# Optimization experiments

Measured on AMD Instinct MI355X. Metric: run time of the kernel, lower is better.

Reference implementation:

```python
import jax, jax.numpy as jnp
import numpy as np

EPS = 1e-12  # torch F.normalize eps

def setup_inputs() -> dict:
    key = jax.random.key(0)
    k1, k2, k3 = jax.random.split(key, 3)
    N, F_IN, F_OUT = 8192, 512, 256
    adjacency = jax.random.uniform(k1, (N, N), dtype=jnp.float32)
    input_feature = jax.random.normal(k2, (N, F_IN), dtype=jnp.float32)
    # xavier_normal_ with gain=1: std = sqrt(2/(fan_in+fan_out))
    std = float(np.sqrt(2.0 / (F_IN + F_OUT)))
    weight = jax.random.normal(k3, (F_IN, F_OUT), dtype=jnp.float32) * std
    bias = jnp.zeros((F_OUT,), dtype=jnp.float32)
    return {"adjacency": adjacency, "input_feature": input_feature,
            "weight": weight, "bias": bias}

def reference(adjacency, input_feature, weight, bias):
    # row L1 normalization, matching torch.nn.functional.normalize(p=1, dim=1)
    row_norm = jnp.sum(jnp.abs(adjacency), axis=1, keepdims=True)
    adj_n = adjacency / jnp.maximum(row_norm, EPS)
    support = adj_n @ input_feature            # [N, F_in]
    output = support @ weight + bias           # [N, F_out]
    return output
```

## Files before the change

kernel.cpp:

```cpp
#include <hip/hip_runtime.h>
#include <hip/hip_bf16.h>


typedef __attribute__((ext_vector_type(8))) __bf16 bf16x8;
typedef __attribute__((ext_vector_type(4))) float f32x4;

#define AS1 __attribute__((address_space(1)))
#define AS3 __attribute__((address_space(3)))

__device__ __forceinline__ void async_load16(const void* g, void* l) {
  __builtin_amdgcn_global_load_lds((const AS1 void*)g, (AS3 void*)l, 16, 0, 0);
}

__global__ __launch_bounds__(256) void transpose_cvt_kernel(
    const float* __restrict__ src, __hip_bfloat16* __restrict__ dst, int R, int C) {
  __shared__ float tile[64][65];
  const int t = threadIdx.x;
  const int nrb = R >> 6;
  const int rb = blockIdx.x % nrb, cb = blockIdx.x / nrb;
  const int r0 = rb * 64, c0 = cb * 64;
  const int lr = t >> 4, lc4 = (t & 15) * 4;
#pragma unroll
  for (int p = 0; p < 4; ++p) {
    const int r = p * 16 + lr;
    const f32x4 v = *(const f32x4*)(src + (size_t)(r0 + r) * C + c0 + lc4);
    tile[r][lc4 + 0] = v[0]; tile[r][lc4 + 1] = v[1];
    tile[r][lc4 + 2] = v[2]; tile[r][lc4 + 3] = v[3];
  }
  __syncthreads();
#pragma unroll
  for (int i = 0; i < 16; ++i) {
    const int idx = i * 256 + t;
    const int n = idx >> 6, k = idx & 63;
    dst[(size_t)(c0 + n) * R + r0 + k] = __float2bfloat16(tile[k][n]);
  }
}

__global__ __launch_bounds__(256) void gemm_xw_kernel(
    const float* __restrict__ X,
    const __hip_bfloat16* __restrict__ WT,
    __hip_bfloat16* __restrict__ YT)
{
  __shared__ char smem[49152];
  char* Sbase = smem;
  char* Wbase = smem + 16384;

  const int t = threadIdx.x;
  const int wave = t >> 6, lane = t & 63;
  const int quad = lane >> 4, l16 = lane & 15;

  const int b = blockIdx.x;
  const int xcd = b & 7, s = b >> 3;
  const int rb = xcd * 16 + (s >> 1), cb = s & 1;
  const int r0 = rb * 64, c0 = cb * 128;

  const int wm = wave & 1, wn = wave >> 1;

  f32x4 acc[2][4] = {};

  const int am = t >> 2;
  const int kq = t & 3;
  const float* sp = X + (size_t)(r0 + am) * 512 + kq * 16;
  const int sw0 = am * 128 + (((kq * 2 + 0) ^ (am & 7)) * 16);
  const int sw1 = am * 128 + (((kq * 2 + 1) ^ (am & 7)) * 16);

  f32x4 sreg[4];
#pragma unroll
  for (int i = 0; i < 4; ++i) sreg[i] = *(const f32x4*)(sp + i * 4);

#pragma unroll
  for (int i = 0; i < 4; ++i) {
    const int slot = i * 256 + t;
    const int n = slot >> 3;
    const int G = (slot & 7) ^ (n & 7);
    async_load16(WT + (size_t)(c0 + n) * 512 + G * 8, Wbase + slot * 16);
  }

  int cur = 0;
#pragma unroll 2
  for (int kt = 0; kt < 8; ++kt) {
    {
      char* sw = Sbase + cur * 8192;
      bf16x8 v0, v1;
#pragma unroll
      for (int j = 0; j < 4; ++j) {
        v0[j]     = (__bf16)(sreg[0][j]);
        v0[j + 4] = (__bf16)(sreg[1][j]);
        v1[j]     = (__bf16)(sreg[2][j]);
        v1[j + 4] = (__bf16)(sreg[3][j]);
      }
      *(bf16x8*)(sw + sw0) = v0;
      *(bf16x8*)(sw + sw1) = v1;
    }
    __syncthreads();

    if (kt < 7) {
      const float* spk = sp + (kt + 1) * 64;
#pragma unroll
      for (int i = 0; i < 4; ++i) sreg[i] = *(const f32x4*)(spk + i * 4);
#pragma unroll
      for (int i = 0; i < 4; ++i) {
        const int slot = i * 256 + t;
        const int n = slot >> 3;
        const int G = (slot & 7) ^ (n & 7);
        async_load16(WT + (size_t)(c0 + n) * 512 + (kt + 1) * 64 + G * 8,
                     Wbase + (cur ^ 1) * 16384 + slot * 16);
      }
    }

    {
      const char* sb = Sbase + cur * 8192;
      const char* wb = Wbase + cur * 16384;
      bf16x8 af[2][2];
#pragma unroll
      for (int rt = 0; rt < 2; ++rt) {
        const int row = wm * 32 + rt * 16 + l16;
#pragma unroll
        for (int kb = 0; kb < 2; ++kb) {
          const int ch = (kb * 4 + quad) ^ (row & 7);
          af[rt][kb] = *(const bf16x8*)(sb + row * 128 + ch * 16);
        }
      }
#pragma unroll
      for (int ct = 0; ct < 4; ++ct) {
        const int n = wn * 64 + ct * 16 + l16;
#pragma unroll
        for (int kb = 0; kb < 2; ++kb) {
          const int ch = (kb * 4 + quad) ^ (n & 7);
          const bf16x8 bfr = *(const bf16x8*)(wb + n * 128 + ch * 16);
#pragma unroll
          for (int rt = 0; rt < 2; ++rt)
            acc[rt][ct] = __builtin_amdgcn_mfma_f32_16x16x32_bf16(
                af[rt][kb], bfr, acc[rt][ct], 0, 0, 0);
        }
      }
    }
    cur ^= 1;
  }

  __syncthreads();
  __hip_bfloat16* Tr = (__hip_bfloat16*)smem;
#pragma unroll
  for (int rt = 0; rt < 2; ++rt) {
#pragma unroll
    for (int r = 0; r < 4; ++r) {
      const int row_l = wm * 32 + rt * 16 + quad * 4 + r;
#pragma unroll
      for (int ct = 0; ct < 4; ++ct) {
        const int col_l = wn * 64 + ct * 16 + l16;
        Tr[col_l * 64 + row_l] = __float2bfloat16(acc[rt][ct][r]);
      }
    }
  }
  __syncthreads();
#pragma unroll
  for (int i = 0; i < 4; ++i) {
    const int c = i * 256 + t;
    const int col = c >> 3, part = c & 7;
    *(f32x4*)(YT + (size_t)(c0 + col) * 8192 + r0 + part * 8) =
        *(const f32x4*)(Tr + col * 64 + part * 8);
  }
}

__global__ __launch_bounds__(512, 4) void gemm_ay_kernel(
    const float* __restrict__ A,
    const __hip_bfloat16* __restrict__ YT,
    float* __restrict__ Pb,
    float* __restrict__ Rb,
    int atomic_flag)
{
  __shared__ char smem[49152];
  char* Abase = smem;
  char* Ybase = smem + 16384;
  float* rsmem = (float*)Ybase;

  const int t = threadIdx.x;
  const int wave = t >> 6, lane = t & 63;
  const int quad = lane >> 4, l16 = lane & 15;

  const int b = blockIdx.x;
  const int ks = b & 7;
  const int rb = b >> 3;
  const int r0 = rb * 128;
  const int k0 = ks * 1024;

  const int wm = wave & 1, wn = wave >> 1;

  f32x4 acc[4][4] = {};
  float rs = 0.0f;

  const int am = t >> 2;
  const int kc = t & 3;
  const float* ap = A + (size_t)(r0 + am) * 8192 + k0 + kc * 8;
  const int aw_off = (am >> 1) * 128 + (((kc + 4 * (am & 1)) ^ ((am >> 1) & 7)) * 16);

  f32x4 areg[2];
  areg[0] = *(const f32x4*)(ap);
  areg[1] = *(const f32x4*)(ap + 4);

#pragma unroll
  for (int i = 0; i < 2; ++i) {
    const int s = i * 512 + t;
    const int q = s >> 3;
    const int u = (s & 7) ^ (q & 7);
    const int n = 2 * q + (u >> 2), g = u & 3;
    async_load16(YT + (size_t)n * 8192 + k0 + g * 8, Ybase + s * 16);
  }

  int cur = 0;
#pragma unroll 2
  for (int kt = 0; kt < 32; ++kt) {
    {
      const f32x4 e = areg[0], o = areg[1];
      rs += fabsf(e[0]) + fabsf(e[1]) + fabsf(e[2]) + fabsf(e[3]) +
            fabsf(o[0]) + fabsf(o[1]) + fabsf(o[2]) + fabsf(o[3]);
      bf16x8 v;
      v[0] = (__bf16)e[0]; v[1] = (__bf16)e[1]; v[2] = (__bf16)e[2]; v[3] = (__bf16)e[3];
      v[4] = (__bf16)o[0]; v[5] = (__bf16)o[1]; v[6] = (__bf16)o[2]; v[7] = (__bf16)o[3];
      *(bf16x8*)(Abase + cur * 8192 + aw_off) = v;
    }
    __syncthreads();

    if (kt < 31) {
      const float* apk = ap + (kt + 1) * 32;
      areg[0] = *(const f32x4*)(apk);
      areg[1] = *(const f32x4*)(apk + 4);
#pragma unroll
      for (int i = 0; i < 2; ++i) {
        const int s = i * 512 + t;
        const int q = s >> 3;
        const int u = (s & 7) ^ (q & 7);
        const int n = 2 * q + (u >> 2), g = u & 3;
        async_load16(YT + (size_t)n * 8192 + k0 + (kt + 1) * 32 + g * 8,
                     Ybase + (cur ^ 1) * 16384 + s * 16);
      }
    }

    {
      const char* ab = Abase + cur * 8192;
      const char* xb = Ybase + cur * 16384;
      bf16x8 af[4];
#pragma unroll
      for (int rt = 0; rt < 4; ++rt) {
        const int row = wm * 64 + rt * 16 + l16;
        const int off = (row >> 1) * 128 + (((quad + 4 * (row & 1)) ^ ((row >> 1) & 7)) * 16);
        af[rt] = *(const bf16x8*)(ab + off);
      }
#pragma unroll
      for (int ct = 0; ct < 4; ++ct) {
        const int n = wn * 64 + ct * 16 + l16;
        const int off = (n >> 1) * 128 + (((quad + 4 * (n & 1)) ^ ((n >> 1) & 7)) * 16);
        const bf16x8 bfr = *(const bf16x8*)(xb + off);
#pragma unroll
        for (int rt = 0; rt < 4; ++rt)
          acc[rt][ct] = __builtin_amdgcn_mfma_f32_16x16x32_bf16(
              af[rt], bfr, acc[rt][ct], 0, 0, 0);
      }
    }
    cur ^= 1;
  }

  rsmem[t] = rs;
  __syncthreads();
  if (t < 128) {
    const float v = rsmem[4 * t] + rsmem[4 * t + 1] + rsmem[4 * t + 2] + rsmem[4 * t + 3];
    if (atomic_flag) atomicAdd(&Rb[r0 + t], v);
    else             Rb[(size_t)ks * 8192 + r0 + t] = v;
  }

  if (atomic_flag) {
#pragma unroll
    for (int rt = 0; rt < 4; ++rt)
#pragma unroll
      for (int r = 0; r < 4; ++r) {
        const int row_l = wm * 64 + rt * 16 + quad * 4 + r;
#pragma unroll
        for (int ct = 0; ct < 4; ++ct) {
          const int col_l = wn * 64 + ct * 16 + l16;
          atomicAdd(&Pb[(size_t)(r0 + row_l) * 256 + col_l], acc[rt][ct][r]);
        }
      }
  } else {
    float* dst = Pb + (size_t)ks * (8192 * 256);
#pragma unroll
    for (int rt = 0; rt < 4; ++rt)
#pragma unroll
      for (int r = 0; r < 4; ++r) {
        const int row_l = wm * 64 + rt * 16 + quad * 4 + r;
#pragma unroll
        for (int ct = 0; ct < 4; ++ct) {
          const int col_l = wn * 64 + ct * 16 + l16;
          dst[(size_t)(r0 + row_l) * 256 + col_l] = acc[rt][ct][r];
        }
      }
  }
}

__global__ __launch_bounds__(256) void finalize_kernel(
    const float* __restrict__ Pb,
    const float* __restrict__ Rb,
    const float* __restrict__ bias,
    float* __restrict__ Out,
    int S)
{
  const int idx = blockIdx.x * 256 + threadIdx.x;
  const int i  = idx >> 6;
  const int j4 = (idx & 63) << 2;
  float rsum = 0.0f;
  for (int s = 0; s < S; ++s) rsum += Rb[(size_t)s * 8192 + i];
  const float inv = 1.0f / fmaxf(rsum, 1e-12f);
  f32x4 a = {};
  for (int s = 0; s < S; ++s) {
    const f32x4 p = *(const f32x4*)(Pb + (size_t)s * (8192 * 256) + (size_t)i * 256 + j4);
    a += p;
  }
  const f32x4 bv = *(const f32x4*)(bias + j4);
  const f32x4 o = a * inv + bv;
  *(f32x4*)(Out + (size_t)i * 256 + j4) = o;
}

extern "C" void kernel_launch(void* const* d_in, const int* in_sizes, int n_in,
                              void* d_out, int out_size, void* d_ws, size_t ws_size,
                              hipStream_t stream) {
  const float* A    = (const float*)d_in[0];
  const float* Xf   = (const float*)d_in[1];
  const float* Wf   = (const float*)d_in[2];
  const float* bias = (const float*)d_in[3];
  float* Out = (float*)d_out;

  char* ws = (char*)d_ws;
  __hip_bfloat16* WT = (__hip_bfloat16*)ws;
  __hip_bfloat16* YT = (__hip_bfloat16*)(ws + 262144);
  char*         tail = ws + 4456448;

  const size_t need_plain = 4456448ull + 67108864ull + 262144ull;
  float* Pb; float* Rb; int atomic_flag; int S;
  if (ws_size >= need_plain) {
    Pb = (float*)tail;
    Rb = (float*)(tail + 67108864);
    atomic_flag = 0; S = 8;
  } else {
    Pb = (float*)tail;
    Rb = (float*)(tail + 8388608);
    atomic_flag = 1; S = 1;
    hipMemsetAsync(tail, 0, 8388608 + 32768, stream);
  }

  transpose_cvt_kernel<<<32, 256, 0, stream>>>(Wf, WT, 512, 256);
  gemm_xw_kernel<<<256, 256, 0, stream>>>(Xf, WT, YT);
  gemm_ay_kernel<<<512, 512, 0, stream>>>(A, YT, Pb, Rb, atomic_flag);
  finalize_kernel<<<2048, 256, 0, stream>>>(Pb, Rb, bias, Out, S);
}
```

Before: 435.1 us.

## Replace split-K A·Y GEMM with full-K tiles and fused normalization epilogue

The big adjacency GEMM no longer splits K across 8 blocks that write fp32 partials into a 64 MB workspace for a separate finalize kernel. Each block now runs the full K=8192 on a 64x128 output tile, reduces row L1 norms in-block, and writes normalized output plus bias directly. The K step grows to 128 with a double-buffered register prefetch of A, and LDS grows to 96 KB. This removes the partial write/read traffic and one launch, but grid size drops to 256 blocks with lower occupancy, and each block rereads A rows for its two column tiles.

```diff
diff --git a/kernel.cpp b/kernel.cpp
--- a/kernel.cpp
+++ b/kernel.cpp
@@ -162,161 +162,140 @@
   }
 }
 
-__global__ __launch_bounds__(512, 4) void gemm_ay_kernel(
+__global__ __launch_bounds__(512, 2) void gemm_ay_kernel(
     const float* __restrict__ A,
     const __hip_bfloat16* __restrict__ YT,
-    float* __restrict__ Pb,
-    float* __restrict__ Rb,
-    int atomic_flag)
+    const float* __restrict__ bias,
+    float* __restrict__ Out)
 {
-  __shared__ char smem[49152];
+  __shared__ char smem[98304];
   char* Abase = smem;
-  char* Ybase = smem + 16384;
-  float* rsmem = (float*)Ybase;
+  char* Ybase = smem + 32768;
 
   const int t = threadIdx.x;
   const int wave = t >> 6, lane = t & 63;
   const int quad = lane >> 4, l16 = lane & 15;
 
   const int b = blockIdx.x;
-  const int ks = b & 7;
-  const int rb = b >> 3;
-  const int r0 = rb * 128;
-  const int k0 = ks * 1024;
+  const int cb = b >> 7, rb = b & 127;
+  const int r0 = rb * 64, c0 = cb * 128;
 
   const int wm = wave & 1, wn = wave >> 1;
 
-  f32x4 acc[4][4] = {};
+  f32x4 acc[2][2] = {};
   float rs = 0.0f;
 
-  const int am = t >> 2;
-  const int kc = t & 3;
-  const float* ap = A + (size_t)(r0 + am) * 8192 + k0 + kc * 8;
-  const int aw_off = (am >> 1) * 128 + (((kc + 4 * (am & 1)) ^ ((am >> 1) & 7)) * 16);
-
-  f32x4 areg[2];
-  areg[0] = *(const f32x4*)(ap);
-  areg[1] = *(const f32x4*)(ap + 4);
-
-#pragma unroll
-  for (int i = 0; i < 2; ++i) {
+  const int am = t >> 3, kc = t & 7;
+  const float* ap = A + (size_t)(r0 + am) * 8192 + kc * 16;
+  const int aw0 = am * 256 + (((2 * kc + 0) ^ (am & 15)) * 16);
+  const int aw1 = am * 256 + (((2 * kc + 1) ^ (am & 15)) * 16);
+
+  f32x4 areg[2][4];
+#pragma unroll
+  for (int i = 0; i < 4; ++i) areg[0][i] = *(const f32x4*)(ap + i * 4);
+#pragma unroll
+  for (int i = 0; i < 4; ++i) areg[1][i] = *(const f32x4*)(ap + 128 + i * 4);
+#pragma unroll
+  for (int i = 0; i < 4; ++i) {
     const int s = i * 512 + t;
-    const int q = s >> 3;
-    const int u = (s & 7) ^ (q & 7);
-    const int n = 2 * q + (u >> 2), g = u & 3;
-    async_load16(YT + (size_t)n * 8192 + k0 + g * 8, Ybase + s * 16);
+    const int n = s >> 4;
+    const int lg = (s & 15) ^ (n & 15);
+    async_load16(YT + (size_t)(c0 + n) * 8192 + lg * 8, Ybase + s * 16);
   }
 
   int cur = 0;
 #pragma unroll 2
-  for (int kt = 0; kt < 32; ++kt) {
+  for (int kt = 0; kt < 64; ++kt) {
     {
-      const f32x4 e = areg[0], o = areg[1];
-      rs += fabsf(e[0]) + fabsf(e[1]) + fabsf(e[2]) + fabsf(e[3]) +
-            fabsf(o[0]) + fabsf(o[1]) + fabsf(o[2]) + fabsf(o[3]);
-      bf16x8 v;
-      v[0] = (__bf16)e[0]; v[1] = (__bf16)e[1]; v[2] = (__bf16)e[2]; v[3] = (__bf16)e[3];
-      v[4] = (__bf16)o[0]; v[5] = (__bf16)o[1]; v[6] = (__bf16)o[2]; v[7] = (__bf16)o[3];
-      *(bf16x8*)(Abase + cur * 8192 + aw_off) = v;
+      const int p = kt & 1;
+      const f32x4 a0 = areg[p][0], a1 = areg[p][1], a2 = areg[p][2], a3 = areg[p][3];
+      rs += fabsf(a0[0]) + fabsf(a0[1]) + fabsf(a0[2]) + fabsf(a0[3]) +
+            fabsf(a1[0]) + fabsf(a1[1]) + fabsf(a1[2]) + fabsf(a1[3]) +
+            fabsf(a2[0]) + fabsf(a2[1]) + fabsf(a2[2]) + fabsf(a2[3]) +
+            fabsf(a3[0]) + fabsf(a3[1]) + fabsf(a3[2]) + fabsf(a3[3]);
+      bf16x8 v0, v1;
+#pragma unroll
+      for (int j = 0; j < 4; ++j) {
+        v0[j] = (__bf16)a0[j]; v0[j + 4] = (__bf16)a1[j];
+        v1[j] = (__bf16)a2[j]; v1[j + 4] = (__bf16)a3[j];
+      }
+      char* aw = Abase + cur * 16384;
+      *(bf16x8*)(aw + aw0) = v0;
+      *(bf16x8*)(aw + aw1) = v1;
     }
     __syncthreads();
 
-    if (kt < 31) {
-      const float* apk = ap + (kt + 1) * 32;
-      areg[0] = *(const f32x4*)(apk);
-      areg[1] = *(const f32x4*)(apk + 4);
-#pragma unroll
-      for (int i = 0; i < 2; ++i) {
+    if (kt < 62) {
+      const float* apk = ap + (size_t)(kt + 2) * 128;
+#pragma unroll
+      for (int i = 0; i < 4; ++i) areg[kt & 1][i] = *(const f32x4*)(apk + i * 4);
+    }
+    if (kt < 63) {
+#pragma unroll
+      for (int i = 0; i < 4; ++i) {
         const int s = i * 512 + t;
-        const int q = s >> 3;
-        const int u = (s & 7) ^ (q & 7);
-        const int n = 2 * q + (u >> 2), g = u & 3;
-        async_load16(YT + (size_t)n * 8192 + k0 + (kt + 1) * 32 + g * 8,
-                     Ybase + (cur ^ 1) * 16384 + s * 16);
+        const int n = s >> 4;
+        const int lg = (s & 15) ^ (n & 15);
+        async_load16(YT + (size_t)(c0 + n) * 8192 + (kt + 1) * 128 + lg * 8,
+                     Ybase + (cur ^ 1) * 32768 + s * 16);
       }
     }
 
     {
-      const char* ab = Abase + cur * 8192;
-      const char* xb = Ybase + cur * 16384;
-      bf16x8 af[4];
-#pragma unroll
-      for (int rt = 0; rt < 4; ++rt) {
-        const int row = wm * 64 + rt * 16 + l16;
-        const int off = (row >> 1) * 128 + (((quad + 4 * (row & 1)) ^ ((row >> 1) & 7)) * 16);
-        af[rt] = *(const bf16x8*)(ab + off);
-      }
-#pragma unroll
-      for (int ct = 0; ct < 4; ++ct) {
-        const int n = wn * 64 + ct * 16 + l16;
-        const int off = (n >> 1) * 128 + (((quad + 4 * (n & 1)) ^ ((n >> 1) & 7)) * 16);
-        const bf16x8 bfr = *(const bf16x8*)(xb + off);
-#pragma unroll
-        for (int rt = 0; rt < 4; ++rt)
-          acc[rt][ct] = __builtin_amdgcn_mfma_f32_16x16x32_bf16(
-              af[rt], bfr, acc[rt][ct], 0, 0, 0);
+      const char* ab = Abase + cur * 16384;
+      const char* yb = Ybase + cur * 32768;
+      bf16x8 af[2][4];
+#pragma unroll
+      for (int rt = 0; rt < 2; ++rt) {
+        const int row = wm * 32 + rt * 16 + l16;
+#pragma unroll
+        for (int kb = 0; kb < 4; ++kb) {
+          const int ch = (kb * 4 + quad) ^ (row & 15);
+          af[rt][kb] = *(const bf16x8*)(ab + row * 256 + ch * 16);
+        }
+      }
+#pragma unroll
+      for (int ct = 0; ct < 2; ++ct) {
+        const int n = wn * 32 + ct * 16 + l16;
+#pragma unroll
+        for (int kb = 0; kb < 4; ++kb) {
+          const int ch = (kb * 4 + quad) ^ (n & 15);
+          const bf16x8 bfr = *(const bf16x8*)(yb + n * 256 + ch * 16);
+#pragma unroll
+          for (int rt = 0; rt < 2; ++rt)
+            acc[rt][ct] = __builtin_amdgcn_mfma_f32_16x16x32_bf16(
+                af[rt][kb], bfr, acc[rt][ct], 0, 0, 0);
+        }
       }
     }
     cur ^= 1;
   }
 
+  float* rsmem = (float*)Abase;
+  float* rinv  = (float*)(Abase + 2048);
   rsmem[t] = rs;
   __syncthreads();
-  if (t < 128) {
-    const float v = rsmem[4 * t] + rsmem[4 * t + 1] + rsmem[4 * t + 2] + rsmem[4 * t + 3];
-    if (atomic_flag) atomicAdd(&Rb[r0 + t], v);
-    else             Rb[(size_t)ks * 8192 + r0 + t] = v;
-  }
-
-  if (atomic_flag) {
-#pragma unroll
-    for (int rt = 0; rt < 4; ++rt)
-#pragma unroll
-      for (int r = 0; r < 4; ++r) {
-        const int row_l = wm * 64 + rt * 16 + quad * 4 + r;
-#pragma unroll
-        for (int ct = 0; ct < 4; ++ct) {
-          const int col_l = wn * 64 + ct * 16 + l16;
-          atomicAdd(&Pb[(size_t)(r0 + row_l) * 256 + col_l], acc[rt][ct][r]);
-        }
-      }
-  } else {
-    float* dst = Pb + (size_t)ks * (8192 * 256);
-#pragma unroll
-    for (int rt = 0; rt < 4; ++rt)
-#pragma unroll
-      for (int r = 0; r < 4; ++r) {
-        const int row_l = wm * 64 + rt * 16 + quad * 4 + r;
-#pragma unroll
-        for (int ct = 0; ct < 4; ++ct) {
-          const int col_l = wn * 64 + ct * 16 + l16;
-          dst[(size_t)(r0 + row_l) * 256 + col_l] = acc[rt][ct][r];
-        }
-      }
-  }
-}
-
-__global__ __launch_bounds__(256) void finalize_kernel(
-    const float* __restrict__ Pb,
-    const float* __restrict__ Rb,
-    const float* __restrict__ bias,
-    float* __restrict__ Out,
-    int S)
-{
-  const int idx = blockIdx.x * 256 + threadIdx.x;
-  const int i  = idx >> 6;
-  const int j4 = (idx & 63) << 2;
-  float rsum = 0.0f;
-  for (int s = 0; s < S; ++s) rsum += Rb[(size_t)s * 8192 + i];
-  const float inv = 1.0f / fmaxf(rsum, 1e-12f);
-  f32x4 a = {};
-  for (int s = 0; s < S; ++s) {
-    const f32x4 p = *(const f32x4*)(Pb + (size_t)s * (8192 * 256) + (size_t)i * 256 + j4);
-    a += p;
-  }
-  const f32x4 bv = *(const f32x4*)(bias + j4);
-  const f32x4 o = a * inv + bv;
-  *(f32x4*)(Out + (size_t)i * 256 + j4) = o;
+  if (t < 64) {
+    float v = 0.0f;
+#pragma unroll
+    for (int j = 0; j < 8; ++j) v += rsmem[t * 8 + j];
+    rinv[t] = 1.0f / fmaxf(v, 1e-12f);
+  }
+  __syncthreads();
+#pragma unroll
+  for (int rt = 0; rt < 2; ++rt) {
+#pragma unroll
+    for (int r = 0; r < 4; ++r) {
+      const int row_l = wm * 32 + rt * 16 + quad * 4 + r;
+      const float inv = rinv[row_l];
+#pragma unroll
+      for (int ct = 0; ct < 2; ++ct) {
+        const int col_l = wn * 32 + ct * 16 + l16;
+        Out[(size_t)(r0 + row_l) * 256 + c0 + col_l] =
+            acc[rt][ct][r] * inv + bias[c0 + col_l];
+      }
+    }
+  }
 }
 
 extern "C" void kernel_launch(void* const* d_in, const int* in_sizes, int n_in,
@@ -331,23 +310,8 @@
   char* ws = (char*)d_ws;
   __hip_bfloat16* WT = (__hip_bfloat16*)ws;
   __hip_bfloat16* YT = (__hip_bfloat16*)(ws + 262144);
-  char*         tail = ws + 4456448;
-
-  const size_t need_plain = 4456448ull + 67108864ull + 262144ull;
-  float* Pb; float* Rb; int atomic_flag; int S;
-  if (ws_size >= need_plain) {
-    Pb = (float*)tail;
-    Rb = (float*)(tail + 67108864);
-    atomic_flag = 0; S = 8;
-  } else {
-    Pb = (float*)tail;
-    Rb = (float*)(tail + 8388608);
-    atomic_flag = 1; S = 1;
-    hipMemsetAsync(tail, 0, 8388608 + 32768, stream);
-  }
 
   transpose_cvt_kernel<<<32, 256, 0, stream>>>(Wf, WT, 512, 256);
   gemm_xw_kernel<<<256, 256, 0, stream>>>(Xf, WT, YT);
-  gemm_ay_kernel<<<512, 512, 0, stream>>>(A, YT, Pb, Rb, atomic_flag);
-  finalize_kernel<<<2048, 256, 0, stream>>>(Pb, Rb, bias, Out, S);
-}
+  gemm_ay_kernel<<<256, 512, 0, stream>>>(A, YT, bias, Out);
+}
```

Result: faster. 418.8 us (-3.8%).

## Deepen A*Y K-tile to 64, halve split-K, stagger K start per row block

Applied to the files above, without the earlier changes.

The big A·Y GEMM now uses a K tile of 64 instead of 32, with 4-way split-K instead of 8-way, so the grid is 256 blocks. Each block walks its K range starting at a rotated phase per row block to spread DRAM and L2 accesses, and prefetches A two tiles ahead in registers. The row-sum reduction now uses lane shuffles instead of shared memory. The changes aim to cut partial-sum traffic and finalize work and to raise MFMA work per barrier, at the cost of doubling LDS to 96KB, lowering occupancy to 2 blocks per CU, and having fewer blocks than before.

```diff
diff --git a/kernel.cpp b/kernel.cpp
--- a/kernel.cpp
+++ b/kernel.cpp
@@ -162,110 +162,130 @@
   }
 }
 
-__global__ __launch_bounds__(512, 4) void gemm_ay_kernel(
+__global__ __launch_bounds__(512, 2) void gemm_ay_kernel(
     const float* __restrict__ A,
     const __hip_bfloat16* __restrict__ YT,
     float* __restrict__ Pb,
     float* __restrict__ Rb,
     int atomic_flag)
 {
-  __shared__ char smem[49152];
+  __shared__ char smem[98304];
   char* Abase = smem;
-  char* Ybase = smem + 16384;
-  float* rsmem = (float*)Ybase;
+  char* Ybase = smem + 32768;
 
   const int t = threadIdx.x;
   const int wave = t >> 6, lane = t & 63;
   const int quad = lane >> 4, l16 = lane & 15;
 
   const int b = blockIdx.x;
-  const int ks = b & 7;
-  const int rb = b >> 3;
+  const int ks = b & 3;
+  const int rb = b >> 2;
   const int r0 = rb * 128;
-  const int k0 = ks * 1024;
+  const int k0 = ks * 2048;
+  const int phase = (rb * 37) & 31;
 
   const int wm = wave & 1, wn = wave >> 1;
 
   f32x4 acc[4][4] = {};
   float rs = 0.0f;
 
-  const int am = t >> 2;
-  const int kc = t & 3;
-  const float* ap = A + (size_t)(r0 + am) * 8192 + k0 + kc * 8;
-  const int aw_off = (am >> 1) * 128 + (((kc + 4 * (am & 1)) ^ ((am >> 1) & 7)) * 16);
-
-  f32x4 areg[2];
-  areg[0] = *(const f32x4*)(ap);
-  areg[1] = *(const f32x4*)(ap + 4);
-
-#pragma unroll
-  for (int i = 0; i < 2; ++i) {
-    const int s = i * 512 + t;
-    const int q = s >> 3;
-    const int u = (s & 7) ^ (q & 7);
-    const int n = 2 * q + (u >> 2), g = u & 3;
-    async_load16(YT + (size_t)n * 8192 + k0 + g * 8, Ybase + s * 16);
+  const int am = t >> 2, kq = t & 3;
+  const float* ap = A + (size_t)(r0 + am) * 8192 + k0 + kq * 16;
+  const int aw0 = am * 128 + (((2 * kq + 0) ^ (am & 7)) * 16);
+  const int aw1 = am * 128 + (((2 * kq + 1) ^ (am & 7)) * 16);
+
+  f32x4 areg[2][4];
+  {
+    const int kk0 = phase, kk1 = (phase + 1) & 31;
+#pragma unroll
+    for (int i = 0; i < 4; ++i) areg[0][i] = *(const f32x4*)(ap + kk0 * 64 + i * 4);
+#pragma unroll
+    for (int i = 0; i < 4; ++i) areg[1][i] = *(const f32x4*)(ap + kk1 * 64 + i * 4);
+#pragma unroll
+    for (int i = 0; i < 4; ++i) {
+      const int s = i * 512 + t;
+      const int n = s >> 3;
+      const int G = (s & 7) ^ (n & 7);
+      async_load16(YT + (size_t)n * 8192 + k0 + kk0 * 64 + G * 8, Ybase + s * 16);
+    }
   }
 
   int cur = 0;
 #pragma unroll 2
   for (int kt = 0; kt < 32; ++kt) {
     {
-      const f32x4 e = areg[0], o = areg[1];
-      rs += fabsf(e[0]) + fabsf(e[1]) + fabsf(e[2]) + fabsf(e[3]) +
-            fabsf(o[0]) + fabsf(o[1]) + fabsf(o[2]) + fabsf(o[3]);
-      bf16x8 v;
-      v[0] = (__bf16)e[0]; v[1] = (__bf16)e[1]; v[2] = (__bf16)e[2]; v[3] = (__bf16)e[3];
-      v[4] = (__bf16)o[0]; v[5] = (__bf16)o[1]; v[6] = (__bf16)o[2]; v[7] = (__bf16)o[3];
-      *(bf16x8*)(Abase + cur * 8192 + aw_off) = v;
+      const int p = kt & 1;
+      const f32x4 a0 = areg[p][0], a1 = areg[p][1], a2 = areg[p][2], a3 = areg[p][3];
+      rs += fabsf(a0[0]) + fabsf(a0[1]) + fabsf(a0[2]) + fabsf(a0[3]) +
+            fabsf(a1[0]) + fabsf(a1[1]) + fabsf(a1[2]) + fabsf(a1[3]) +
+            fabsf(a2[0]) + fabsf(a2[1]) + fabsf(a2[2]) + fabsf(a2[3]) +
+            fabsf(a3[0]) + fabsf(a3[1]) + fabsf(a3[2]) + fabsf(a3[3]);
+      bf16x8 v0, v1;
+#pragma unroll
+      for (int j = 0; j < 4; ++j) {
+        v0[j] = (__bf16)a0[j]; v0[j + 4] = (__bf16)a1[j];
+        v1[j] = (__bf16)a2[j]; v1[j + 4] = (__bf16)a3[j];
+      }
+      char* aw = Abase + cur * 16384;
+      *(bf16x8*)(aw + aw0) = v0;
+      *(bf16x8*)(aw + aw1) = v1;
     }
     __syncthreads();
 
+    if (kt < 30) {
+      const int kk2 = (kt + 2 + phase) & 31;
+      const float* apk = ap + (size_t)kk2 * 64;
+#pragma unroll
+      for (int i = 0; i < 4; ++i) areg[kt & 1][i] = *(const f32x4*)(apk + i * 4);
+    }
     if (kt < 31) {
-      const float* apk = ap + (kt + 1) * 32;
-      areg[0] = *(const f32x4*)(apk);
-      areg[1] = *(const f32x4*)(apk + 4);
-#pragma unroll
-      for (int i = 0; i < 2; ++i) {
+      const int kk1 = (kt + 1 + phase) & 31;
+#pragma unroll
+      for (int i = 0; i < 4; ++i) {
         const int s = i * 512 + t;
-        const int q = s >> 3;
-        const int u = (s & 7) ^ (q & 7);
-        const int n = 2 * q + (u >> 2), g = u & 3;
-        async_load16(YT + (size_t)n * 8192 + k0 + (kt + 1) * 32 + g * 8,
-                     Ybase + (cur ^ 1) * 16384 + s * 16);
+        const int n = s >> 3;
+        const int G = (s & 7) ^ (n & 7);
+        async_load16(YT + (size_t)n * 8192 + k0 + kk1 * 64 + G * 8,
+                     Ybase + (cur ^ 1) * 32768 + s * 16);
       }
     }
 
     {
-      const char* ab = Abase + cur * 8192;
-      const char* xb = Ybase + cur * 16384;
-      bf16x8 af[4];
+      const char* ab = Abase + cur * 16384;
+      const char* yb = Ybase + cur * 32768;
+      bf16x8 af[4][2];
 #pragma unroll
       for (int rt = 0; rt < 4; ++rt) {
         const int row = wm * 64 + rt * 16 + l16;
-        const int off = (row >> 1) * 128 + (((quad + 4 * (row & 1)) ^ ((row >> 1) & 7)) * 16);
-        af[rt] = *(const bf16x8*)(ab + off);
+#pragma unroll
+        for (int kb = 0; kb < 2; ++kb) {
+          const int ch = (kb * 4 + quad) ^ (row & 7);
+          af[rt][kb] = *(const bf16x8*)(ab + row * 128 + ch * 16);
+        }
       }
 #pragma unroll
       for (int ct = 0; ct < 4; ++ct) {
         const int n = wn * 64 + ct * 16 + l16;
-        const int off = (n >> 1) * 128 + (((quad + 4 * (n & 1)) ^ ((n >> 1) & 7)) * 16);
-        const bf16x8 bfr = *(const bf16x8*)(xb + off);
-#pragma unroll
-        for (int rt = 0; rt < 4; ++rt)
-          acc[rt][ct] = __builtin_amdgcn_mfma_f32_16x16x32_bf16(
-              af[rt], bfr, acc[rt][ct], 0, 0, 0);
+#pragma unroll
+        for (int kb = 0; kb < 2; ++kb) {
+          const int ch = (kb * 4 + quad) ^ (n & 7);
+          const bf16x8 bfr = *(const bf16x8*)(yb + n * 128 + ch * 16);
+#pragma unroll
+          for (int rt = 0; rt < 4; ++rt)
+            acc[rt][ct] = __builtin_amdgcn_mfma_f32_16x16x32_bf16(
+                af[rt][kb], bfr, acc[rt][ct], 0, 0, 0);
+        }
       }
     }
     cur ^= 1;
   }
 
-  rsmem[t] = rs;
-  __syncthreads();
-  if (t < 128) {
-    const float v = rsmem[4 * t] + rsmem[4 * t + 1] + rsmem[4 * t + 2] + rsmem[4 * t + 3];
-    if (atomic_flag) atomicAdd(&Rb[r0 + t], v);
-    else             Rb[(size_t)ks * 8192 + r0 + t] = v;
+  rs += __shfl_xor(rs, 1);
+  rs += __shfl_xor(rs, 2);
+  if ((t & 3) == 0) {
+    const int row = t >> 2;
+    if (atomic_flag) atomicAdd(&Rb[r0 + row], rs);
+    else             Rb[(size_t)ks * 8192 + r0 + row] = rs;
   }
 
   if (atomic_flag) {
@@ -333,12 +353,12 @@
   __hip_bfloat16* YT = (__hip_bfloat16*)(ws + 262144);
   char*         tail = ws + 4456448;
 
-  const size_t need_plain = 4456448ull + 67108864ull + 262144ull;
+  const size_t need_plain = 4456448ull + 33554432ull + 131072ull;
   float* Pb; float* Rb; int atomic_flag; int S;
   if (ws_size >= need_plain) {
     Pb = (float*)tail;
-    Rb = (float*)(tail + 67108864);
-    atomic_flag = 0; S = 8;
+    Rb = (float*)(tail + 33554432);
+    atomic_flag = 0; S = 4;
   } else {
     Pb = (float*)tail;
     Rb = (float*)(tail + 8388608);
@@ -348,6 +368,6 @@
 
   transpose_cvt_kernel<<<32, 256, 0, stream>>>(Wf, WT, 512, 256);
   gemm_xw_kernel<<<256, 256, 0, stream>>>(Xf, WT, YT);
-  gemm_ay_kernel<<<512, 512, 0, stream>>>(A, YT, Pb, Rb, atomic_flag);
+  gemm_ay_kernel<<<256, 512, 0, stream>>>(A, YT, Pb, Rb, atomic_flag);
   finalize_kernel<<<2048, 256, 0, stream>>>(Pb, Rb, bias, Out, S);
 }
```

After: 399.3 us. 1.09x faster.
